# Optimization experiments

Hardware: AMD Instinct MI355X
Metric: run time of the kernel (lower is better)

## Reference

```python
import jax, jax.numpy as jnp
import numpy as np

B, H, W, C = 8, 64, 64, 128
L = H * W
NH = 4
HD = C // NH
SCALE = HD ** -0.5
WIN = 8
SHIFT = 4
DEPTH = 2
K = 3
N = WIN * WIN
NW = (H // WIN) * (W // WIN)


def _rel_pos_index(win):
    coords = np.stack(np.meshgrid(np.arange(win), np.arange(win), indexing='ij'))
    cf = coords.reshape(2, -1)
    rel = (cf[:, :, None] - cf[:, None, :]).transpose(1, 2, 0).copy()
    rel[:, :, 0] += win - 1
    rel[:, :, 1] += win - 1
    rel[:, :, 0] *= 2 * win - 1
    return rel.sum(-1)  # (N, N)

REL_IDX = jnp.asarray(_rel_pos_index(WIN).reshape(-1))


def _attn_mask(Hh, Ww, win, shift):
    img = np.zeros((Hh, Ww))
    cnt = 0
    for hs in (slice(0, -win), slice(-win, -shift), slice(-shift, None)):
        for ws in (slice(0, -win), slice(-win, -shift), slice(-shift, None)):
            img[hs, ws] = cnt
            cnt += 1
    mw = img.reshape(Hh // win, win, Ww // win, win).transpose(0, 2, 1, 3).reshape(-1, win * win)
    m = mw[:, None, :] - mw[:, :, None]
    return jnp.asarray(np.where(m != 0, -100.0, 0.0).astype(np.float32))  # (nW, N, N)

ATTN_MASK = _attn_mask(H, W, WIN, SHIFT)


def layer_norm(x, g, b, eps=1e-5):
    mu = x.mean(-1, keepdims=True)
    var = x.var(-1, keepdims=True)
    return (x - mu) / jnp.sqrt(var + eps) * g + b


def window_partition(x, win):
    Bb, Hh, Ww, Cc = x.shape
    x = x.reshape(Bb, Hh // win, win, Ww // win, win, Cc)
    return x.transpose(0, 1, 3, 2, 4, 5).reshape(-1, win, win, Cc)


def window_reverse(wins, win, Hh, Ww):
    Bb = wins.shape[0] // (Hh * Ww // win // win)
    x = wins.reshape(Bb, Hh // win, Ww // win, win, win, -1)
    return x.transpose(0, 1, 3, 2, 4, 5).reshape(Bb, Hh, Ww, -1)


def swin_block(x, shift, n1g, n1b, qkvw, qkvb, rp, pw, pb, n2g, n2b, f1w, f1b, f2w, f2b):
    shortcut = x
    x = layer_norm(x, n1g, n1b).reshape(B, H, W, C)
    if shift > 0:
        x = jnp.roll(x, (-shift, -shift), axis=(1, 2))
    xw = window_partition(x, WIN).reshape(-1, N, C)  # (B*nW, N, C)
    qkv = (xw @ qkvw + qkvb).reshape(-1, N, 3, NH, HD).transpose(2, 0, 3, 1, 4)
    q, k, v = qkv[0] * SCALE, qkv[1], qkv[2]
    attn = jnp.einsum('whnd,whmd->whnm', q, k)  # (B*nW, NH, N, N)
    bias = rp[REL_IDX].reshape(N, N, NH).transpose(2, 0, 1)
    attn = attn + bias[None]
    if shift > 0:
        attn = (attn.reshape(B, NW, NH, N, N) + ATTN_MASK[None, :, None]).reshape(-1, NH, N, N)
    attn = jax.nn.softmax(attn, axis=-1)
    out = jnp.einsum('whnm,whmd->whnd', attn, v).transpose(0, 2, 1, 3).reshape(-1, N, C)
    out = out @ pw + pb
    x = window_reverse(out.reshape(-1, WIN, WIN, C), WIN, H, W)
    if shift > 0:
        x = jnp.roll(x, (shift, shift), axis=(1, 2))
    x = shortcut + x.reshape(B, L, C)
    h = layer_norm(x, n2g, n2b)
    h = jax.nn.gelu(h @ f1w + f1b, approximate=False) @ f2w + f2b
    return x + h


def conv1d(x, w, b):  # x (B,C,L), w (O,I,K)
    y = jax.lax.conv_general_dilated(x, w, (1,), [(K // 2, K // 2)], dimension_numbers=('NCH', 'OIH', 'NCH'))
    return y + b[None, :, None]


def deform_conv1d(xt, off_w, off_b, msk_w, msk_b):
    x = xt.transpose(0, 2, 1)  # (B, C, L)
    offset = conv1d(x, off_w, off_b)                    # (B, K, L)
    mask = jax.nn.sigmoid(conv1d(x, msk_w, msk_b))      # (B, K, L)
    i = jnp.arange(L, dtype=x.dtype)
    pos = jnp.clip(i[None, None, :] + offset, 0.0, L - 1)  # (B, K, L)
    fp = jnp.floor(pos).astype(jnp.int32)
    cp = jnp.minimum(fp + 1, L - 1)
    alpha = pos - fp.astype(x.dtype)
    idx_f = jnp.broadcast_to(fp[:, None], (B, C, K, L))
    idx_c = jnp.broadcast_to(cp[:, None], (B, C, K, L))
    xe = jnp.broadcast_to(x[:, :, None, :], (B, C, K, L))
    xf = jnp.take_along_axis(xe, idx_f, axis=3)
    xc = jnp.take_along_axis(xe, idx_c, axis=3)
    samp = xf * (1.0 - alpha[:, None]) + xc * alpha[:, None]
    out = (samp * mask[:, None]).sum(2)  # (B, C, L)
    # faithful to torch: output.view(B, L, out_channels) reinterprets memory, no transpose
    return out.reshape(B, L, C)


def _forward(xt, hx, cx, red_w, red_b, n1g, n1b, qkvw, qkvb, rp, pw, pb, n2g, n2b,
             f1w, f1b, f2w, f2b, off_w, off_b, msk_w, msk_b, lf_w, lf_b, gf_w, gf_b, ff_w, ff_b):
    # global branch: inject hidden state then W-MSA / SW-MSA blocks
    g = jnp.concatenate([xt, hx], axis=-1) @ red_w + red_b
    for i, shift in enumerate((0, SHIFT)):
        g = swin_block(g, shift, n1g[i], n1b[i], qkvw[i], qkvb[i], rp[i], pw[i], pb[i],
                       n2g[i], n2b[i], f1w[i], f1b[i], f2w[i], f2b[i])
    # local branch: deformable 1D conv over token axis
    local = deform_conv1d(xt, off_w, off_b, msk_w, msk_b)
    # local-global fusion
    fu = jax.nn.relu((local @ lf_w + lf_b) * (g @ gf_w + gf_b)) @ ff_w + ff_b
    # LSTM-style gating (SwinLSTM cell update)
    gate = jax.nn.sigmoid(fu)
    cell = jnp.tanh(fu)
    cy = gate * (cx + cell)
    hy = gate * jnp.tanh(cy)
    return hy


def setup_inputs():
    key = jax.random.key(0)
    ks = iter(jax.random.split(key, 24))
    def rn(shape, s=0.02):
        return jax.random.normal(next(ks), shape, jnp.float32) * s
    return dict(
        xt=jax.random.normal(next(ks), (B, L, C), jnp.float32),
        hx=jax.random.normal(next(ks), (B, L, C), jnp.float32),
        cx=jax.random.normal(next(ks), (B, L, C), jnp.float32),
        red_w=rn((2 * C, C)), red_b=jnp.zeros((C,), jnp.float32),
        n1g=jnp.ones((DEPTH, C), jnp.float32), n1b=jnp.zeros((DEPTH, C), jnp.float32),
        qkvw=rn((DEPTH, C, 3 * C)), qkvb=jnp.zeros((DEPTH, 3 * C), jnp.float32),
        rp=rn((DEPTH, (2 * WIN - 1) ** 2, NH)),
        pw=rn((DEPTH, C, C)), pb=jnp.zeros((DEPTH, C), jnp.float32),
        n2g=jnp.ones((DEPTH, C), jnp.float32), n2b=jnp.zeros((DEPTH, C), jnp.float32),
        f1w=rn((DEPTH, C, 4 * C)), f1b=jnp.zeros((DEPTH, 4 * C), jnp.float32),
        f2w=rn((DEPTH, 4 * C, C)), f2b=jnp.zeros((DEPTH, C), jnp.float32),
        off_w=rn((K, C, K)), off_b=jnp.zeros((K,), jnp.float32),
        msk_w=rn((K, C, K)), msk_b=jnp.zeros((K,), jnp.float32),
        lf_w=rn((C, C)), lf_b=jnp.zeros((C,), jnp.float32),
        gf_w=rn((C, C)), gf_b=jnp.zeros((C,), jnp.float32),
        ff_w=rn((C, C)), ff_b=jnp.zeros((C,), jnp.float32),
    )


def reference(xt, hx, cx, red_w, red_b, n1g, n1b, qkvw, qkvb, rp, pw, pb, n2g, n2b,
              f1w, f1b, f2w, f2b, off_w, off_b, msk_w, msk_b, lf_w, lf_b, gf_w, gf_b, ff_w, ff_b):
    return _forward(xt, hx, cx, red_w, red_b, n1g, n1b, qkvw, qkvb, rp, pw, pb, n2g, n2b,
                    f1w, f1b, f2w, f2b, off_w, off_b, msk_w, msk_b, lf_w, lf_b, gf_w, gf_b, ff_w, ff_b)
```

## Files before the change

### kernel.cpp

```cpp
#include <hip/hip_runtime.h>
#include <hip/hip_bf16.h>
#include <math.h>

typedef __hip_bfloat16 bf16;
typedef unsigned short u16;
#define BF(x) __bfloat162float(x)
static __device__ __forceinline__ bf16 FB(float x) { return __float2bfloat16(x); }
static __device__ __forceinline__ u16 FBu(float x) {
    bf16 b = __float2bfloat16(x);
    return *(u16*)&b;
}

typedef __attribute__((ext_vector_type(4))) float f32x4;
typedef __attribute__((ext_vector_type(8))) __bf16 bf16x8;


#define O_REDW 0
#define O_QKVW 32768
#define O_PW   131072
#define O_F1W  163840
#define O_F2W  294912
#define O_LFW  425984
#define O_GFW  442368
#define O_FFW  458752
#define O_REDB 475136
#define O_QKVB 475264
#define O_PB   476032
#define O_F1B  476288
#define O_F2B  477312
#define O_LFB  477568
#define O_GFB  477696
#define O_FFB  477824
#define O_RP   477952
#define O_N1G  479752
#define O_N1B  480008
#define O_N2G  480264
#define O_N2B  480520
#define O_OW   480776
#define O_OB   481928
#define O_MW   481931
#define O_MB   483083

#define ROW_S 36
#define CH_S  2320

__device__ __forceinline__ int get_mode(const void* xt) {
    const unsigned* w = (const unsigned*)xt;
    int zlo = 0, inband = 0;
    #pragma unroll
    for (int i = 0; i < 32; ++i) {
        unsigned lo = w[i] & 0xFFFFu;
        int e = (int)((lo >> 7) & 0xFF);
        zlo += (lo == 0u || lo == 0x8000u);
        inband += (e >= 100 && e <= 140);
    }
    if (zlo >= 29) return 1;
    return (inband >= 20) ? 0 : 1;
}

__device__ __forceinline__ float LD(const void* p, size_t i, int mode) {
    return mode ? ((const float*)p)[i] : BF(((const bf16*)p)[i]);
}

__device__ __forceinline__ void async16(const u16* g, u16* l) {
    __builtin_amdgcn_global_load_lds(
        (const __attribute__((address_space(1))) unsigned int*)g,
        (__attribute__((address_space(3))) unsigned int*)l, 16, 0, 0);
}

struct PrepT { const void* src; int srcOff, K, N, dstOff; };
struct Prep { PrepT d[29]; int start[30]; };

__global__ void prep_k(Prep p, bf16* __restrict__ dst, const void* __restrict__ dtp) {
    const int mode = get_mode(dtp);
    int i = blockIdx.x * 256 + threadIdx.x;
    if (i >= p.start[29]) return;
    int s = 0;
    while (p.start[s + 1] <= i) ++s;
    int e = i - p.start[s];
    float v;
    if (p.d[s].N > 0) {
        int n = e / p.d[s].K, k = e % p.d[s].K;
        v = LD(p.d[s].src, (size_t)p.d[s].srcOff + (size_t)k * p.d[s].N + n, mode);
    } else {
        v = LD(p.d[s].src, (size_t)p.d[s].srcOff + e, mode);
    }
    dst[p.d[s].dstOff + e] = FB(v);
}

__launch_bounds__(256)
__global__ void xcat_k(const void* __restrict__ xt, const void* __restrict__ hx,
                       u16* __restrict__ X) {
    const int mode = get_mode(xt);
    const int total = 32768 * 32;
    for (int gidx = blockIdx.x * 256 + threadIdx.x; gidx < total;
         gidx += gridDim.x * 256) {
        int r = gidx >> 5, gi = gidx & 31;
        const void* src = (gi < 16) ? xt : hx;
        int c = (gi & 15) << 3;
        u16 outv[8];
        if (mode) {
            const float* s = (const float*)src + (size_t)r * 128 + c;
            float4 a = *(const float4*)s;
            float4 b = *(const float4*)(s + 4);
            outv[0] = FBu(a.x); outv[1] = FBu(a.y); outv[2] = FBu(a.z); outv[3] = FBu(a.w);
            outv[4] = FBu(b.x); outv[5] = FBu(b.y); outv[6] = FBu(b.z); outv[7] = FBu(b.w);
        } else {
            *(uint4*)outv = *(const uint4*)((const u16*)src + (size_t)r * 128 + c);
        }
        *(uint4*)(X + (size_t)r * 256 + (gi << 3)) = *(const uint4*)outv;
    }
}

template <int EPI>
__launch_bounds__(256)
__global__ void gemm_mfma(const u16* __restrict__ A, const u16* __restrict__ Bt,
                          const bf16* __restrict__ bias, bf16* __restrict__ outb,
                          float* __restrict__ outf, int M, int N, int K, int shift) {
    __shared__ __align__(16) u16 Als[4096];
    __shared__ __align__(16) u16 Bls[4096];
    const int tid = threadIdx.x;
    const int wave = tid >> 6, lane = tid & 63;
    const int q = lane >> 4, lr = lane & 15;
    const int wm = (wave >> 1) << 6, wn = (wave & 1) << 6;
    const int bm = blockIdx.y << 7, bn = blockIdx.x << 7;
    const f32x4 zero = {0.f, 0.f, 0.f, 0.f};
    f32x4 acc[4][4];
    #pragma unroll
    for (int i = 0; i < 4; ++i)
        #pragma unroll
        for (int j = 0; j < 4; ++j) acc[i][j] = zero;

    for (int k0 = 0; k0 < K; k0 += 32) {
        #pragma unroll
        for (int c = tid; c < 512; c += 256) {
            async16(A + (size_t)(bm + (c >> 2)) * K + k0 + ((c & 3) << 3), Als + (c << 3));
            async16(Bt + (size_t)(bn + (c >> 2)) * K + k0 + ((c & 3) << 3), Bls + (c << 3));
        }
        __syncthreads();
        bf16x8 af[4], bfr[4];
        #pragma unroll
        for (int t = 0; t < 4; ++t) {
            af[t]  = *(const bf16x8*)(Als + ((wm + (t << 4) + lr) << 5) + (q << 3));
            bfr[t] = *(const bf16x8*)(Bls + ((wn + (t << 4) + lr) << 5) + (q << 3));
        }
        #pragma unroll
        for (int mt = 0; mt < 4; ++mt)
            #pragma unroll
            for (int nt = 0; nt < 4; ++nt)
                acc[mt][nt] = __builtin_amdgcn_mfma_f32_16x16x32_bf16(
                    af[mt], bfr[nt], acc[mt][nt], 0, 0, 0);
        __syncthreads();
    }

    #pragma unroll
    for (int nt = 0; nt < 4; ++nt) {
        int col = bn + wn + (nt << 4) + lr;
        float bv = BF(bias[col]);
        #pragma unroll
        for (int mt = 0; mt < 4; ++mt) {
            int row0 = bm + wm + (mt << 4) + (q << 2);
            #pragma unroll
            for (int i = 0; i < 4; ++i) {
                int r = row0 + i;
                float v = acc[mt][nt][i] + bv;
                size_t idx = (size_t)r * N + col;
                if (EPI == 0) {
                    outb[idx] = FB(v);
                } else if (EPI == 3) {
                    int b = r >> 12, rem = r & 4095;
                    int wi = rem >> 6, n = rem & 63;
                    int hp = ((wi >> 3) << 3) + (n >> 3);
                    int wp = ((wi & 7) << 3) + (n & 7);
                    int h = (hp + shift) & 63, w = (wp + shift) & 63;
                    outf[((size_t)((b << 12) + (h << 6) + w)) * 128 + col] += v;
                } else if (EPI == 5) {
                    outf[idx] = v;
                }
            }
        }
    }
}

__launch_bounds__(256)
__global__ void qkvln_k(const float* __restrict__ g, const u16* __restrict__ wtu,
                        const bf16* __restrict__ wtb, u16* __restrict__ qkv,
                        int d, int shift) {
    __shared__ __align__(16) u16 Ach[4 * CH_S];
    __shared__ __align__(16) u16 Bb[16384];
    const int tid = threadIdx.x;
    const int wave = tid >> 6, lane = tid & 63;
    const int q = lane >> 4, lr = lane & 15;
    const int wm = (wave >> 1) << 5, wn = (wave & 1) << 6;
    const int bm = blockIdx.x << 6;

    {
        int row = tid >> 2, qtr = tid & 3;
        int r = bm + row;
        int b = r >> 12, rem = r & 4095;
        int wi = rem >> 6, n = rem & 63;
        int hp = ((wi >> 3) << 3) + (n >> 3);
        int wp = ((wi & 7) << 3) + (n & 7);
        int h = (hp + shift) & 63, w = (wp + shift) & 63;
        int src = (b << 12) + (h << 6) + w;
        const float* gr = g + (size_t)src * 128 + qtr * 32;
        float vals[32];
        float s1 = 0.f, s2 = 0.f;
        #pragma unroll
        for (int i = 0; i < 8; ++i) {
            float4 v4 = *(const float4*)(gr + i * 4);
            vals[i * 4] = v4.x; vals[i * 4 + 1] = v4.y;
            vals[i * 4 + 2] = v4.z; vals[i * 4 + 3] = v4.w;
            s1 += v4.x + v4.y + v4.z + v4.w;
            s2 += v4.x * v4.x + v4.y * v4.y + v4.z * v4.z + v4.w * v4.w;
        }
        s1 += __shfl_xor(s1, 1); s1 += __shfl_xor(s1, 2);
        s2 += __shfl_xor(s2, 1); s2 += __shfl_xor(s2, 2);
        float mu = s1 * (1.f / 128.f);
        float var = s2 * (1.f / 128.f) - mu * mu;
        float inv = rsqrtf(var + 1e-5f);
        #pragma unroll
        for (int i = 0; i < 32; ++i) {
            int c = qtr * 32 + i;
            float o = (vals[i] - mu) * inv * BF(wtb[O_N1G + d * 128 + c])
                      + BF(wtb[O_N1B + d * 128 + c]);
            Ach[qtr * CH_S + row * ROW_S + i] = FBu(o);
        }
    }
    __syncthreads();

    const f32x4 zero = {0.f, 0.f, 0.f, 0.f};
    for (int nc = 0; nc < 3; ++nc) {
        const u16* Bg = wtu + O_QKVW + d * 49152 + nc * 16384;
        #pragma unroll
        for (int i = tid; i < 2048; i += 256) {
            int kc = i >> 9, c = i & 511;
            async16(Bg + (size_t)(c >> 2) * 128 + (kc << 5) + ((c & 3) << 3),
                    Bb + (kc << 12) + (c << 3));
        }
        __syncthreads();
        f32x4 acc[2][4];
        #pragma unroll
        for (int i = 0; i < 2; ++i)
            #pragma unroll
            for (int j = 0; j < 4; ++j) acc[i][j] = zero;
        #pragma unroll
        for (int k0 = 0; k0 < 4; ++k0) {
            bf16x8 af[2], bfr[4];
            #pragma unroll
            for (int t = 0; t < 2; ++t)
                af[t] = *(const bf16x8*)(Ach + k0 * CH_S + (wm + (t << 4) + lr) * ROW_S + (q << 3));
            #pragma unroll
            for (int t = 0; t < 4; ++t)
                bfr[t] = *(const bf16x8*)(Bb + (k0 << 12) + ((wn + (t << 4) + lr) << 5) + (q << 3));
            #pragma unroll
            for (int mt = 0; mt < 2; ++mt)
                #pragma unroll
                for (int nt = 0; nt < 4; ++nt)
                    acc[mt][nt] = __builtin_amdgcn_mfma_f32_16x16x32_bf16(
                        af[mt], bfr[nt], acc[mt][nt], 0, 0, 0);
        }
        #pragma unroll
        for (int nt = 0; nt < 4; ++nt) {
            int col = wn + (nt << 4) + lr;
            float bv = BF(wtb[O_QKVB + d * 384 + nc * 128 + col]);
            #pragma unroll
            for (int mt = 0; mt < 2; ++mt) {
                #pragma unroll
                for (int i = 0; i < 4; ++i) {
                    int r = bm + wm + (mt << 4) + (q << 2) + i;
                    qkv[(size_t)r * 384 + nc * 128 + col] = FBu(acc[mt][nt][i] + bv);
                }
            }
        }
        __syncthreads();
    }
}

__launch_bounds__(256)
__global__ void attn_k(const u16* __restrict__ qkv, const bf16* __restrict__ rp,
                       u16* __restrict__ outp, int shift) {
    __shared__ float kT[4][32][64];
    __shared__ float vT[4][32][64];
    const int wq = blockIdx.x;
    const int head = threadIdx.x >> 6;
    const int t = threadIdx.x & 63;
    const size_t rbase = (size_t)(wq * 64 + t) * 384 + head * 32;
    float q[32];
    #pragma unroll
    for (int j = 0; j < 4; ++j) {
        bf16x8 qv = *(const bf16x8*)(qkv + rbase + j * 8);
        bf16x8 kv = *(const bf16x8*)(qkv + rbase + 128 + j * 8);
        bf16x8 vv = *(const bf16x8*)(qkv + rbase + 256 + j * 8);
        #pragma unroll
        for (int e = 0; e < 8; ++e) {
            int dd = j * 8 + e;
            q[dd] = (float)qv[e] * 0.17677669529663687f;
            kT[head][dd][t] = (float)kv[e];
            vT[head][dd][t] = (float)vv[e];
        }
    }
    __syncthreads();
    const int wloc = wq & 63;
    const int wh = (wloc >> 3) << 3, wwb = (wloc & 7) << 3;
    int regt = 0;
    if (shift) {
        int hp = wh + (t >> 3), wp = wwb + (t & 7);
        int rh = hp < 56 ? 0 : (hp < 60 ? 1 : 2);
        int rw = wp < 56 ? 0 : (wp < 60 ? 1 : 2);
        regt = rh * 3 + rw;
    }
    const int ti = t >> 3, tj = t & 7;
    float s[64];
    float mx = -1e30f;
    #pragma unroll
    for (int m = 0; m < 64; ++m) {
        float acc = 0.f;
        #pragma unroll
        for (int dd = 0; dd < 32; ++dd) acc += q[dd] * kT[head][dd][m];
        int idx = (ti - (m >> 3) + 7) * 15 + (tj - (m & 7) + 7);
        acc += BF(rp[idx * 4 + head]);
        if (shift) {
            int hp = wh + (m >> 3), wp = wwb + (m & 7);
            int rh = hp < 56 ? 0 : (hp < 60 ? 1 : 2);
            int rw = wp < 56 ? 0 : (wp < 60 ? 1 : 2);
            if (regt != rh * 3 + rw) acc -= 100.f;
        }
        s[m] = acc;
        mx = fmaxf(mx, acc);
    }
    float l = 0.f;
    #pragma unroll
    for (int m = 0; m < 64; ++m) {
        s[m] = expf(s[m] - mx);
        l += s[m];
    }
    const float inv = 1.f / l;
    const size_t obase = (size_t)(wq * 64 + t) * 128 + head * 32;
    #pragma unroll
    for (int j = 0; j < 4; ++j) {
        bf16x8 ov;
        #pragma unroll
        for (int e = 0; e < 8; ++e) {
            int dd = j * 8 + e;
            float a = 0.f;
            #pragma unroll
            for (int m = 0; m < 64; ++m) a += s[m] * vT[head][dd][m];
            ov[e] = (__bf16)(a * inv);
        }
        *(bf16x8*)(outp + obase + j * 8) = ov;
    }
}

__launch_bounds__(256)
__global__ void mlp_k(float* __restrict__ g, bf16* __restrict__ gbf,
                      const u16* __restrict__ wtu, const bf16* __restrict__ wtb,
                      int d) {
    __shared__ __align__(16) u16 Ach[4 * CH_S];
    __shared__ __align__(16) u16 buf1[8192];
    __shared__ __align__(16) u16 buf2[2 * CH_S];
    const int tid = threadIdx.x;
    const int wave = tid >> 6, lane = tid & 63;
    const int q = lane >> 4, lr = lane & 15;
    const int wm = (wave >> 1) << 5;
    const int wn0 = (wave & 1) << 5;
    const int wn = (wave & 1) << 6;
    const int bm = blockIdx.x << 6;

    {
        int row = tid >> 2, qtr = tid & 3;
        const float* gr = g + (size_t)(bm + row) * 128 + qtr * 32;
        float vals[32];
        float s1 = 0.f, s2 = 0.f;
        #pragma unroll
        for (int i = 0; i < 8; ++i) {
            float4 v4 = *(const float4*)(gr + i * 4);
            vals[i * 4] = v4.x; vals[i * 4 + 1] = v4.y;
            vals[i * 4 + 2] = v4.z; vals[i * 4 + 3] = v4.w;
            s1 += v4.x + v4.y + v4.z + v4.w;
            s2 += v4.x * v4.x + v4.y * v4.y + v4.z * v4.z + v4.w * v4.w;
        }
        s1 += __shfl_xor(s1, 1); s1 += __shfl_xor(s1, 2);
        s2 += __shfl_xor(s2, 1); s2 += __shfl_xor(s2, 2);
        float mu = s1 * (1.f / 128.f);
        float var = s2 * (1.f / 128.f) - mu * mu;
        float inv = rsqrtf(var + 1e-5f);
        #pragma unroll
        for (int i = 0; i < 32; ++i) {
            int c = qtr * 32 + i;
            float o = (vals[i] - mu) * inv * BF(wtb[O_N2G + d * 128 + c])
                      + BF(wtb[O_N2B + d * 128 + c]);
            Ach[qtr * CH_S + row * ROW_S + i] = FBu(o);
        }
    }
    __syncthreads();

    const f32x4 zero = {0.f, 0.f, 0.f, 0.f};
    f32x4 acc2[2][4];
    #pragma unroll
    for (int i = 0; i < 2; ++i)
        #pragma unroll
        for (int j = 0; j < 4; ++j) acc2[i][j] = zero;

    for (int h = 0; h < 8; ++h) {
        const u16* B1g = wtu + O_F1W + d * 65536 + h * 8192;
        #pragma unroll
        for (int i = tid; i < 1024; i += 256) {
            int kc = i >> 8, c = i & 255;
            async16(B1g + (c >> 2) * 128 + (kc << 5) + ((c & 3) << 3),
                    buf1 + (kc << 11) + (c << 3));
        }
        __syncthreads();
        f32x4 acc1[2][2];
        #pragma unroll
        for (int i = 0; i < 2; ++i) { acc1[i][0] = zero; acc1[i][1] = zero; }
        #pragma unroll
        for (int k0 = 0; k0 < 4; ++k0) {
            bf16x8 af[2], bfr[2];
            #pragma unroll
            for (int t = 0; t < 2; ++t) {
                af[t]  = *(const bf16x8*)(Ach + k0 * CH_S + (wm + (t << 4) + lr) * ROW_S + (q << 3));
                bfr[t] = *(const bf16x8*)(buf1 + (k0 << 11) + ((wn0 + (t << 4) + lr) << 5) + (q << 3));
            }
            #pragma unroll
            for (int mt = 0; mt < 2; ++mt)
                #pragma unroll
                for (int nt = 0; nt < 2; ++nt)
                    acc1[mt][nt] = __builtin_amdgcn_mfma_f32_16x16x32_bf16(
                        af[mt], bfr[nt], acc1[mt][nt], 0, 0, 0);
        }
        #pragma unroll
        for (int nt = 0; nt < 2; ++nt) {
            int c = wn0 + (nt << 4) + lr;
            float hb = BF(wtb[O_F1B + d * 512 + h * 64 + c]);
            #pragma unroll
            for (int mt = 0; mt < 2; ++mt) {
                #pragma unroll
                for (int i = 0; i < 4; ++i) {
                    int r = wm + (mt << 4) + (q << 2) + i;
                    float v = acc1[mt][nt][i] + hb;
                    float ge = 0.5f * v * (1.0f + erff(v * 0.70710678118654752f));
                    buf2[(c >> 5) * CH_S + r * ROW_S + (c & 31)] = FBu(ge);
                }
            }
        }
        __syncthreads();
        const u16* B2g = wtu + O_F2W + d * 65536 + h * 64;
        #pragma unroll
        for (int i = tid; i < 1024; i += 256) {
            int kc = i >> 9, c = i & 511;
            async16(B2g + (size_t)(c >> 2) * 512 + (kc << 5) + ((c & 3) << 3),
                    buf1 + (kc << 12) + (c << 3));
        }
        __syncthreads();
        #pragma unroll
        for (int kc = 0; kc < 2; ++kc) {
            bf16x8 ah[2], b2[4];
            #pragma unroll
            for (int t = 0; t < 2; ++t)
                ah[t] = *(const bf16x8*)(buf2 + kc * CH_S + (wm + (t << 4) + lr) * ROW_S + (q << 3));
            #pragma unroll
            for (int t = 0; t < 4; ++t)
                b2[t] = *(const bf16x8*)(buf1 + (kc << 12) + ((wn + (t << 4) + lr) << 5) + (q << 3));
            #pragma unroll
            for (int mt = 0; mt < 2; ++mt)
                #pragma unroll
                for (int nt = 0; nt < 4; ++nt)
                    acc2[mt][nt] = __builtin_amdgcn_mfma_f32_16x16x32_bf16(
                        ah[mt], b2[nt], acc2[mt][nt], 0, 0, 0);
        }
        __syncthreads();
    }
    #pragma unroll
    for (int nt = 0; nt < 4; ++nt) {
        int col = wn + (nt << 4) + lr;
        float bv = BF(wtb[O_F2B + d * 128 + col]);
        #pragma unroll
        for (int mt = 0; mt < 2; ++mt) {
            #pragma unroll
            for (int i = 0; i < 4; ++i) {
                int r = bm + wm + (mt << 4) + (q << 2) + i;
                size_t idx = (size_t)r * 128 + col;
                float nv = g[idx] + acc2[mt][nt][i] + bv;
                g[idx] = nv;
                gbf[idx] = FB(nv);
            }
        }
    }
}

__launch_bounds__(256)
__global__ void fuse3_k(const u16* __restrict__ Aloc, const u16* __restrict__ Ag,
                        const u16* __restrict__ wtu, const bf16* __restrict__ wtb,
                        const void* __restrict__ cx, void* __restrict__ out,
                        const void* __restrict__ dtp) {
    __shared__ __align__(16) u16 sm[32768];
    u16* sA  = sm;
    u16* sG  = sm + 4096;
    u16* sLF = sm + 8192;
    u16* sGF = sm + 12288;
    u16* relb = sm + 16384;
    const int mode = get_mode(dtp);
    const int tid = threadIdx.x;
    const int wave = tid >> 6, lane = tid & 63;
    const int q = lane >> 4, lr = lane & 15;
    const int wm = (wave >> 1) << 6, wn = (wave & 1) << 6;
    const int bm = blockIdx.x << 7;
    const f32x4 zero = {0.f, 0.f, 0.f, 0.f};
    f32x4 acc1[4][4], acc2[4][4];
    #pragma unroll
    for (int i = 0; i < 4; ++i)
        #pragma unroll
        for (int j = 0; j < 4; ++j) { acc1[i][j] = zero; acc2[i][j] = zero; }

    #pragma unroll
    for (int k0 = 0; k0 < 4; ++k0) {
        #pragma unroll
        for (int i = tid; i < 512; i += 256) {
            int ld = i & 63, r0 = (i >> 6) << 4;
            int row = r0 + (ld >> 2), sub = (ld & 3) << 3;
            int dstoff = (r0 << 5) + (ld << 3);
            async16(Aloc + (size_t)(bm + row) * 128 + (k0 << 5) + sub, sA + dstoff);
            async16(Ag   + (size_t)(bm + row) * 128 + (k0 << 5) + sub, sG + dstoff);
            async16(wtu + O_LFW + row * 128 + (k0 << 5) + sub, sLF + dstoff);
            async16(wtu + O_GFW + row * 128 + (k0 << 5) + sub, sGF + dstoff);
        }
        __syncthreads();
        bf16x8 al[4], ag[4], blf[4], bgf[4];
        #pragma unroll
        for (int t = 0; t < 4; ++t) {
            int ro = ((wm + (t << 4) + lr) << 5) + (q << 3);
            int co = ((wn + (t << 4) + lr) << 5) + (q << 3);
            al[t]  = *(const bf16x8*)(sA + ro);
            ag[t]  = *(const bf16x8*)(sG + ro);
            blf[t] = *(const bf16x8*)(sLF + co);
            bgf[t] = *(const bf16x8*)(sGF + co);
        }
        #pragma unroll
        for (int mt = 0; mt < 4; ++mt)
            #pragma unroll
            for (int nt = 0; nt < 4; ++nt) {
                acc1[mt][nt] = __builtin_amdgcn_mfma_f32_16x16x32_bf16(
                    al[mt], blf[nt], acc1[mt][nt], 0, 0, 0);
                acc2[mt][nt] = __builtin_amdgcn_mfma_f32_16x16x32_bf16(
                    ag[mt], bgf[nt], acc2[mt][nt], 0, 0, 0);
            }
        __syncthreads();
    }
    #pragma unroll
    for (int nt = 0; nt < 4; ++nt) {
        int c = wn + (nt << 4) + lr;
        float lfb = BF(wtb[O_LFB + c]);
        float gfb = BF(wtb[O_GFB + c]);
        #pragma unroll
        for (int mt = 0; mt < 4; ++mt) {
            #pragma unroll
            for (int i = 0; i < 4; ++i) {
                int r = wm + (mt << 4) + (q << 2) + i;
                float t1 = acc1[mt][nt][i] + lfb;
                float t2 = acc2[mt][nt][i] + gfb;
                float rel = t1 * t2;
                relb[((c >> 5) << 12) + (r << 5) + (c & 31)] = FBu(rel > 0.f ? rel : 0.f);
            }
        }
    }
    __syncthreads();
    f32x4 acc3[4][4];
    #pragma unroll
    for (int i = 0; i < 4; ++i)
        #pragma unroll
        for (int j = 0; j < 4; ++j) acc3[i][j] = zero;
    #pragma unroll
    for (int k0 = 0; k0 < 4; ++k0) {
        #pragma unroll
        for (int i = tid; i < 512; i += 256) {
            int ld = i & 63, r0 = (i >> 6) << 4;
            int row = r0 + (ld >> 2), sub = (ld & 3) << 3;
            async16(wtu + O_FFW + row * 128 + (k0 << 5) + sub, sA + (r0 << 5) + (ld << 3));
        }
        __syncthreads();
        bf16x8 ar[4], bff[4];
        #pragma unroll
        for (int t = 0; t < 4; ++t) {
            ar[t]  = *(const bf16x8*)(relb + (k0 << 12) + ((wm + (t << 4) + lr) << 5) + (q << 3));
            bff[t] = *(const bf16x8*)(sA + ((wn + (t << 4) + lr) << 5) + (q << 3));
        }
        #pragma unroll
        for (int mt = 0; mt < 4; ++mt)
            #pragma unroll
            for (int nt = 0; nt < 4; ++nt)
                acc3[mt][nt] = __builtin_amdgcn_mfma_f32_16x16x32_bf16(
                    ar[mt], bff[nt], acc3[mt][nt], 0, 0, 0);
        __syncthreads();
    }
    #pragma unroll
    for (int nt = 0; nt < 4; ++nt) {
        int col = wn + (nt << 4) + lr;
        float ffb = BF(wtb[O_FFB + col]);
        #pragma unroll
        for (int mt = 0; mt < 4; ++mt) {
            #pragma unroll
            for (int i = 0; i < 4; ++i) {
                int r = bm + wm + (mt << 4) + (q << 2) + i;
                size_t idx = (size_t)r * 128 + col;
                float v = acc3[mt][nt][i] + ffb;
                float gate = 1.f / (1.f + expf(-v));
                float cell = tanhf(v);
                float cy = gate * (LD(cx, idx, mode) + cell);
                float hy = gate * tanhf(cy);
                if (mode) ((float*)out)[idx] = hy;
                else      ((bf16*)out)[idx] = FB(hy);
            }
        }
    }
}

__launch_bounds__(256)
__global__ void deform_k(const void* __restrict__ xt, const bf16* __restrict__ wtb,
                         bf16* __restrict__ outL) {
    __shared__ __align__(16) u16 ot[128 * 72];
    __shared__ int s_fp[192], s_cp[192];
    __shared__ float s_al[192], s_mk[192];
    const int mode = get_mode(xt);
    const int tid = threadIdx.x;
    const int wave = tid >> 6, lane = tid & 63;
    const int b = blockIdx.x >> 6;
    const int l0 = (blockIdx.x & 63) << 6;
    float wo[3][3][2], wmk[3][3][2];
    #pragma unroll
    for (int k = 0; k < 3; ++k)
        #pragma unroll
        for (int j = 0; j < 3; ++j) {
            wo[k][j][0]  = BF(wtb[O_OW + (k * 128 + lane) * 3 + j]);
            wo[k][j][1]  = BF(wtb[O_OW + (k * 128 + lane + 64) * 3 + j]);
            wmk[k][j][0] = BF(wtb[O_MW + (k * 128 + lane) * 3 + j]);
            wmk[k][j][1] = BF(wtb[O_MW + (k * 128 + lane + 64) * 3 + j]);
        }
    for (int il = 0; il < 16; ++il) {
        int l_loc = wave * 16 + il;
        int l = l0 + l_loc;
        float a6[6] = {};
        #pragma unroll
        for (int j = 0; j < 3; ++j) {
            int row = l + j - 1;
            if (row >= 0 && row < 4096) {
                size_t base = ((size_t)(b << 12) + row) * 128;
                float x0 = LD(xt, base + lane, mode);
                float x1 = LD(xt, base + lane + 64, mode);
                #pragma unroll
                for (int k = 0; k < 3; ++k) {
                    a6[k]     += x0 * wo[k][j][0]  + x1 * wo[k][j][1];
                    a6[3 + k] += x0 * wmk[k][j][0] + x1 * wmk[k][j][1];
                }
            }
        }
        #pragma unroll
        for (int off = 32; off > 0; off >>= 1)
            #pragma unroll
            for (int k = 0; k < 6; ++k) a6[k] += __shfl_down(a6[k], off);
        if (lane == 0) {
            #pragma unroll
            for (int k = 0; k < 3; ++k) {
                float off = a6[k] + BF(wtb[O_OB + k]);
                float pos = fminf(fmaxf((float)l + off, 0.f), 4095.f);
                float fpf = floorf(pos);
                int fp = (int)fpf;
                int cp = fp + 1 > 4095 ? 4095 : fp + 1;
                s_fp[l_loc * 3 + k] = fp;
                s_cp[l_loc * 3 + k] = cp;
                s_al[l_loc * 3 + k] = pos - fpf;
                float mv = a6[3 + k] + BF(wtb[O_MB + k]);
                s_mk[l_loc * 3 + k] = 1.f / (1.f + expf(-mv));
            }
        }
    }
    __syncthreads();
    {
        int c = tid & 127, lh = tid >> 7;
        for (int it = 0; it < 32; ++it) {
            int l_loc = lh * 32 + it;
            float o = 0.f;
            #pragma unroll
            for (int k = 0; k < 3; ++k) {
                int fp = s_fp[l_loc * 3 + k];
                int cp = s_cp[l_loc * 3 + k];
                float al = s_al[l_loc * 3 + k];
                float mk = s_mk[l_loc * 3 + k];
                float xf = LD(xt, ((size_t)(b << 12) + fp) * 128 + c, mode);
                float xc = LD(xt, ((size_t)(b << 12) + cp) * 128 + c, mode);
                o += (xf * (1.f - al) + xc * al) * mk;
            }
            ot[c * 72 + l_loc] = FBu(o);
        }
    }
    __syncthreads();
    #pragma unroll
    for (int pass = 0; pass < 4; ++pass) {
        int cc = pass * 32 + (tid >> 3);
        int oo = tid & 7;
        const uint4 v = *(const uint4*)(ot + cc * 72 + oo * 8);
        *(uint4*)(outL + (size_t)b * 524288 + (size_t)cc * 4096 + l0 + oo * 8) = v;
    }
}

extern "C" void kernel_launch(void* const* d_in, const int* in_sizes, int n_in,
                              void* d_out, int out_size, void* d_ws, size_t ws_size,
                              hipStream_t stream) {
    (void)out_size; (void)ws_size;
    int I[28] = {0,1,2,3,4,5,6,7,8,9,10,11,12,13,14,15,16,17,18,19,20,21,22,23,24,25,26,27};
    if (n_in >= 28 && in_sizes[7] != 98304 && in_sizes[23] == 98304 && in_sizes[26] == 1800) {
        int alt[28] = {27, 9, 0, 25, 24, 15, 14, 23, 22, 26, 21, 20, 17, 16,
                       2, 1, 4, 3, 19, 18, 13, 12, 11, 10, 8, 7, 6, 5};
        for (int i = 0; i < 28; ++i) I[i] = alt[i];
    }
    const void* xt = d_in[I[0]];
    const void* hx = d_in[I[1]];
    const void* cx = d_in[I[2]];

    char* wsb = (char*)d_ws;
    float* g    = (float*)wsb;
    u16*   Abf  = (u16*)(wsb + 16777216);
    u16*   Bbf  = (u16*)(wsb + 25165824);
    u16*   Cbf  = (u16*)(wsb + 50331648);
    bf16*  wtb  = (bf16*)(wsb + 58720256);
    u16*   wtu  = (u16*)wtb;

    Prep p;
    PrepT descs[29] = {
        {d_in[I[3]],  0,     256, 128, O_REDW},
        {d_in[I[7]],  0,     128, 384, O_QKVW},
        {d_in[I[7]],  49152, 128, 384, O_QKVW + 49152},
        {d_in[I[10]], 0,     128, 128, O_PW},
        {d_in[I[10]], 16384, 128, 128, O_PW + 16384},
        {d_in[I[14]], 0,     128, 512, O_F1W},
        {d_in[I[14]], 65536, 128, 512, O_F1W + 65536},
        {d_in[I[16]], 0,     512, 128, O_F2W},
        {d_in[I[16]], 65536, 512, 128, O_F2W + 65536},
        {d_in[I[22]], 0,     128, 128, O_LFW},
        {d_in[I[24]], 0,     128, 128, O_GFW},
        {d_in[I[26]], 0,     128, 128, O_FFW},
        {d_in[I[4]],  0,  128, 0, O_REDB},
        {d_in[I[8]],  0,  768, 0, O_QKVB},
        {d_in[I[11]], 0,  256, 0, O_PB},
        {d_in[I[15]], 0, 1024, 0, O_F1B},
        {d_in[I[17]], 0,  256, 0, O_F2B},
        {d_in[I[23]], 0,  128, 0, O_LFB},
        {d_in[I[25]], 0,  128, 0, O_GFB},
        {d_in[I[27]], 0,  128, 0, O_FFB},
        {d_in[I[9]],  0, 1800, 0, O_RP},
        {d_in[I[5]],  0,  256, 0, O_N1G},
        {d_in[I[6]],  0,  256, 0, O_N1B},
        {d_in[I[12]], 0,  256, 0, O_N2G},
        {d_in[I[13]], 0,  256, 0, O_N2B},
        {d_in[I[18]], 0, 1152, 0, O_OW},
        {d_in[I[19]], 0,    3, 0, O_OB},
        {d_in[I[20]], 0, 1152, 0, O_MW},
        {d_in[I[21]], 0,    3, 0, O_MB},
    };
    int cum = 0;
    for (int i = 0; i < 29; ++i) {
        p.d[i] = descs[i];
        p.start[i] = cum;
        cum += (descs[i].N > 0) ? descs[i].K * descs[i].N : descs[i].K;
    }
    p.start[29] = cum;

    prep_k<<<(cum + 255) / 256, 256, 0, stream>>>(p, wtb, xt);
    xcat_k<<<1024, 256, 0, stream>>>(xt, hx, Bbf);

    gemm_mfma<5><<<dim3(1, 256), 256, 0, stream>>>(Bbf, wtu + O_REDW, wtb + O_REDB,
                                                   nullptr, g, 32768, 128, 256, 0);

    for (int d = 0; d < 2; ++d) {
        int shift = d ? 4 : 0;
        qkvln_k<<<512, 256, 0, stream>>>(g, wtu, wtb, Bbf, d, shift);
        attn_k<<<512, 256, 0, stream>>>(Bbf, wtb + O_RP + d * 900, Cbf, shift);
        gemm_mfma<3><<<dim3(1, 256), 256, 0, stream>>>(Cbf, wtu + O_PW + d * 16384,
                                                       wtb + O_PB + d * 128, nullptr, g,
                                                       32768, 128, 128, shift);
        mlp_k<<<512, 256, 0, stream>>>(g, (bf16*)Abf, wtu, wtb, d);
    }

    deform_k<<<512, 256, 0, stream>>>(xt, wtb, (bf16*)Cbf);
    fuse3_k<<<256, 256, 0, stream>>>(Cbf, Abf, wtu, wtb, cx, d_out, xt);
}
```

Baseline: 459.6 us.

## Load GEMM operands directly from global memory instead of staging through LDS

Removes the async LDS staging and barriers for weight and activation tiles in gemm_mfma, qkvln_k, mlp_k and fuse3_k, so MFMA operand fragments are read straight from global memory through the caches. fuse3_k is also retiled from 128-row to 64-row blocks with a padded LDS layout, launch bounds of 2 blocks per SM and twice as many blocks. The aim is to cut LDS traffic and synchronization and to raise occupancy. The cost is strided uncoalesced 16-byte global loads with no reuse across waves except through L1/L2, which may increase memory latency stalls.

```diff
diff --git a/kernel.cpp b/kernel.cpp
--- a/kernel.cpp
+++ b/kernel.cpp
@@ -117,8 +117,6 @@
 __global__ void gemm_mfma(const u16* __restrict__ A, const u16* __restrict__ Bt,
                           const bf16* __restrict__ bias, bf16* __restrict__ outb,
                           float* __restrict__ outf, int M, int N, int K, int shift) {
-    __shared__ __align__(16) u16 Als[4096];
-    __shared__ __align__(16) u16 Bls[4096];
     const int tid = threadIdx.x;
     const int wave = tid >> 6, lane = tid & 63;
     const int q = lane >> 4, lr = lane & 15;
@@ -132,17 +130,11 @@
         for (int j = 0; j < 4; ++j) acc[i][j] = zero;
 
     for (int k0 = 0; k0 < K; k0 += 32) {
-        #pragma unroll
-        for (int c = tid; c < 512; c += 256) {
-            async16(A + (size_t)(bm + (c >> 2)) * K + k0 + ((c & 3) << 3), Als + (c << 3));
-            async16(Bt + (size_t)(bn + (c >> 2)) * K + k0 + ((c & 3) << 3), Bls + (c << 3));
-        }
-        __syncthreads();
         bf16x8 af[4], bfr[4];
         #pragma unroll
         for (int t = 0; t < 4; ++t) {
-            af[t]  = *(const bf16x8*)(Als + ((wm + (t << 4) + lr) << 5) + (q << 3));
-            bfr[t] = *(const bf16x8*)(Bls + ((wn + (t << 4) + lr) << 5) + (q << 3));
+            af[t]  = *(const bf16x8*)(A  + (size_t)(bm + wm + (t << 4) + lr) * K + k0 + (q << 3));
+            bfr[t] = *(const bf16x8*)(Bt + (size_t)(bn + wn + (t << 4) + lr) * K + k0 + (q << 3));
         }
         #pragma unroll
         for (int mt = 0; mt < 4; ++mt)
@@ -150,7 +142,6 @@
             for (int nt = 0; nt < 4; ++nt)
                 acc[mt][nt] = __builtin_amdgcn_mfma_f32_16x16x32_bf16(
                     af[mt], bfr[nt], acc[mt][nt], 0, 0, 0);
-        __syncthreads();
     }
 
     #pragma unroll
@@ -187,7 +178,6 @@
                         const bf16* __restrict__ wtb, u16* __restrict__ qkv,
                         int d, int shift) {
     __shared__ __align__(16) u16 Ach[4 * CH_S];
-    __shared__ __align__(16) u16 Bb[16384];
     const int tid = threadIdx.x;
     const int wave = tid >> 6, lane = tid & 63;
     const int q = lane >> 4, lr = lane & 15;
@@ -232,13 +222,6 @@
     const f32x4 zero = {0.f, 0.f, 0.f, 0.f};
     for (int nc = 0; nc < 3; ++nc) {
         const u16* Bg = wtu + O_QKVW + d * 49152 + nc * 16384;
-        #pragma unroll
-        for (int i = tid; i < 2048; i += 256) {
-            int kc = i >> 9, c = i & 511;
-            async16(Bg + (size_t)(c >> 2) * 128 + (kc << 5) + ((c & 3) << 3),
-                    Bb + (kc << 12) + (c << 3));
-        }
-        __syncthreads();
         f32x4 acc[2][4];
         #pragma unroll
         for (int i = 0; i < 2; ++i)
@@ -252,7 +235,7 @@
                 af[t] = *(const bf16x8*)(Ach + k0 * CH_S + (wm + (t << 4) + lr) * ROW_S + (q << 3));
             #pragma unroll
             for (int t = 0; t < 4; ++t)
-                bfr[t] = *(const bf16x8*)(Bb + (k0 << 12) + ((wn + (t << 4) + lr) << 5) + (q << 3));
+                bfr[t] = *(const bf16x8*)(Bg + ((wn + (t << 4) + lr) << 7) + (k0 << 5) + (q << 3));
             #pragma unroll
             for (int mt = 0; mt < 2; ++mt)
                 #pragma unroll
@@ -273,7 +256,6 @@
                 }
             }
         }
-        __syncthreads();
     }
 }
 
@@ -357,7 +339,6 @@
                       const u16* __restrict__ wtu, const bf16* __restrict__ wtb,
                       int d) {
     __shared__ __align__(16) u16 Ach[4 * CH_S];
-    __shared__ __align__(16) u16 buf1[8192];
     __shared__ __align__(16) u16 buf2[2 * CH_S];
     const int tid = threadIdx.x;
     const int wave = tid >> 6, lane = tid & 63;
@@ -404,13 +385,6 @@
 
     for (int h = 0; h < 8; ++h) {
         const u16* B1g = wtu + O_F1W + d * 65536 + h * 8192;
-        #pragma unroll
-        for (int i = tid; i < 1024; i += 256) {
-            int kc = i >> 8, c = i & 255;
-            async16(B1g + (c >> 2) * 128 + (kc << 5) + ((c & 3) << 3),
-                    buf1 + (kc << 11) + (c << 3));
-        }
-        __syncthreads();
         f32x4 acc1[2][2];
         #pragma unroll
         for (int i = 0; i < 2; ++i) { acc1[i][0] = zero; acc1[i][1] = zero; }
@@ -420,7 +394,7 @@
             #pragma unroll
             for (int t = 0; t < 2; ++t) {
                 af[t]  = *(const bf16x8*)(Ach + k0 * CH_S + (wm + (t << 4) + lr) * ROW_S + (q << 3));
-                bfr[t] = *(const bf16x8*)(buf1 + (k0 << 11) + ((wn0 + (t << 4) + lr) << 5) + (q << 3));
+                bfr[t] = *(const bf16x8*)(B1g + ((wn0 + (t << 4) + lr) << 7) + (k0 << 5) + (q << 3));
             }
             #pragma unroll
             for (int mt = 0; mt < 2; ++mt)
@@ -447,13 +421,6 @@
         __syncthreads();
         const u16* B2g = wtu + O_F2W + d * 65536 + h * 64;
         #pragma unroll
-        for (int i = tid; i < 1024; i += 256) {
-            int kc = i >> 9, c = i & 511;
-            async16(B2g + (size_t)(c >> 2) * 512 + (kc << 5) + ((c & 3) << 3),
-                    buf1 + (kc << 12) + (c << 3));
-        }
-        __syncthreads();
-        #pragma unroll
         for (int kc = 0; kc < 2; ++kc) {
             bf16x8 ah[2], b2[4];
             #pragma unroll
@@ -461,7 +428,7 @@
                 ah[t] = *(const bf16x8*)(buf2 + kc * CH_S + (wm + (t << 4) + lr) * ROW_S + (q << 3));
             #pragma unroll
             for (int t = 0; t < 4; ++t)
-                b2[t] = *(const bf16x8*)(buf1 + (kc << 12) + ((wn + (t << 4) + lr) << 5) + (q << 3));
+                b2[t] = *(const bf16x8*)(B2g + (size_t)(wn + (t << 4) + lr) * 512 + (kc << 5) + (q << 3));
             #pragma unroll
             for (int mt = 0; mt < 2; ++mt)
                 #pragma unroll
@@ -489,55 +456,42 @@
     }
 }
 
-__launch_bounds__(256)
+__launch_bounds__(256, 2)
 __global__ void fuse3_k(const u16* __restrict__ Aloc, const u16* __restrict__ Ag,
                         const u16* __restrict__ wtu, const bf16* __restrict__ wtb,
                         const void* __restrict__ cx, void* __restrict__ out,
                         const void* __restrict__ dtp) {
-    __shared__ __align__(16) u16 sm[32768];
-    u16* sA  = sm;
-    u16* sG  = sm + 4096;
-    u16* sLF = sm + 8192;
-    u16* sGF = sm + 12288;
-    u16* relb = sm + 16384;
+    __shared__ __align__(16) u16 relb[4 * CH_S];
     const int mode = get_mode(dtp);
     const int tid = threadIdx.x;
     const int wave = tid >> 6, lane = tid & 63;
     const int q = lane >> 4, lr = lane & 15;
-    const int wm = (wave >> 1) << 6, wn = (wave & 1) << 6;
-    const int bm = blockIdx.x << 7;
+    const int wm = (wave >> 1) << 5, wn = (wave & 1) << 6;
+    const int bm = blockIdx.x << 6;
     const f32x4 zero = {0.f, 0.f, 0.f, 0.f};
-    f32x4 acc1[4][4], acc2[4][4];
-    #pragma unroll
-    for (int i = 0; i < 4; ++i)
+    f32x4 acc1[2][4], acc2[2][4];
+    #pragma unroll
+    for (int i = 0; i < 2; ++i)
         #pragma unroll
         for (int j = 0; j < 4; ++j) { acc1[i][j] = zero; acc2[i][j] = zero; }
 
     #pragma unroll
     for (int k0 = 0; k0 < 4; ++k0) {
-        #pragma unroll
-        for (int i = tid; i < 512; i += 256) {
-            int ld = i & 63, r0 = (i >> 6) << 4;
-            int row = r0 + (ld >> 2), sub = (ld & 3) << 3;
-            int dstoff = (r0 << 5) + (ld << 3);
-            async16(Aloc + (size_t)(bm + row) * 128 + (k0 << 5) + sub, sA + dstoff);
-            async16(Ag   + (size_t)(bm + row) * 128 + (k0 << 5) + sub, sG + dstoff);
-            async16(wtu + O_LFW + row * 128 + (k0 << 5) + sub, sLF + dstoff);
-            async16(wtu + O_GFW + row * 128 + (k0 << 5) + sub, sGF + dstoff);
-        }
-        __syncthreads();
-        bf16x8 al[4], ag[4], blf[4], bgf[4];
+        bf16x8 al[2], ag[2], blf[4], bgf[4];
+        #pragma unroll
+        for (int t = 0; t < 2; ++t) {
+            size_t off = (size_t)(bm + wm + (t << 4) + lr) * 128 + (k0 << 5) + (q << 3);
+            al[t] = *(const bf16x8*)(Aloc + off);
+            ag[t] = *(const bf16x8*)(Ag + off);
+        }
         #pragma unroll
         for (int t = 0; t < 4; ++t) {
-            int ro = ((wm + (t << 4) + lr) << 5) + (q << 3);
-            int co = ((wn + (t << 4) + lr) << 5) + (q << 3);
-            al[t]  = *(const bf16x8*)(sA + ro);
-            ag[t]  = *(const bf16x8*)(sG + ro);
-            blf[t] = *(const bf16x8*)(sLF + co);
-            bgf[t] = *(const bf16x8*)(sGF + co);
-        }
-        #pragma unroll
-        for (int mt = 0; mt < 4; ++mt)
+            int woff = ((wn + (t << 4) + lr) << 7) + (k0 << 5) + (q << 3);
+            blf[t] = *(const bf16x8*)(wtu + O_LFW + woff);
+            bgf[t] = *(const bf16x8*)(wtu + O_GFW + woff);
+        }
+        #pragma unroll
+        for (int mt = 0; mt < 2; ++mt)
             #pragma unroll
             for (int nt = 0; nt < 4; ++nt) {
                 acc1[mt][nt] = __builtin_amdgcn_mfma_f32_16x16x32_bf16(
@@ -545,7 +499,6 @@
                 acc2[mt][nt] = __builtin_amdgcn_mfma_f32_16x16x32_bf16(
                     ag[mt], bgf[nt], acc2[mt][nt], 0, 0, 0);
             }
-        __syncthreads();
     }
     #pragma unroll
     for (int nt = 0; nt < 4; ++nt) {
@@ -553,52 +506,45 @@
         float lfb = BF(wtb[O_LFB + c]);
         float gfb = BF(wtb[O_GFB + c]);
         #pragma unroll
-        for (int mt = 0; mt < 4; ++mt) {
+        for (int mt = 0; mt < 2; ++mt) {
             #pragma unroll
             for (int i = 0; i < 4; ++i) {
                 int r = wm + (mt << 4) + (q << 2) + i;
                 float t1 = acc1[mt][nt][i] + lfb;
                 float t2 = acc2[mt][nt][i] + gfb;
                 float rel = t1 * t2;
-                relb[((c >> 5) << 12) + (r << 5) + (c & 31)] = FBu(rel > 0.f ? rel : 0.f);
+                relb[(c >> 5) * CH_S + r * ROW_S + (c & 31)] = FBu(rel > 0.f ? rel : 0.f);
             }
         }
     }
     __syncthreads();
-    f32x4 acc3[4][4];
-    #pragma unroll
-    for (int i = 0; i < 4; ++i)
+    f32x4 acc3[2][4];
+    #pragma unroll
+    for (int i = 0; i < 2; ++i)
         #pragma unroll
         for (int j = 0; j < 4; ++j) acc3[i][j] = zero;
     #pragma unroll
     for (int k0 = 0; k0 < 4; ++k0) {
-        #pragma unroll
-        for (int i = tid; i < 512; i += 256) {
-            int ld = i & 63, r0 = (i >> 6) << 4;
-            int row = r0 + (ld >> 2), sub = (ld & 3) << 3;
-            async16(wtu + O_FFW + row * 128 + (k0 << 5) + sub, sA + (r0 << 5) + (ld << 3));
-        }
-        __syncthreads();
-        bf16x8 ar[4], bff[4];
-        #pragma unroll
-        for (int t = 0; t < 4; ++t) {
-            ar[t]  = *(const bf16x8*)(relb + (k0 << 12) + ((wm + (t << 4) + lr) << 5) + (q << 3));
-            bff[t] = *(const bf16x8*)(sA + ((wn + (t << 4) + lr) << 5) + (q << 3));
-        }
-        #pragma unroll
-        for (int mt = 0; mt < 4; ++mt)
+        bf16x8 ar[2], bff[4];
+        #pragma unroll
+        for (int t = 0; t < 2; ++t)
+            ar[t] = *(const bf16x8*)(relb + k0 * CH_S + (wm + (t << 4) + lr) * ROW_S + (q << 3));
+        #pragma unroll
+        for (int t = 0; t < 4; ++t)
+            bff[t] = *(const bf16x8*)(wtu + O_FFW + ((wn + (t << 4) + lr) << 7) + (k0 << 5) + (q << 3));
+        #pragma unroll
+        for (int mt = 0; mt < 2; ++mt)
             #pragma unroll
             for (int nt = 0; nt < 4; ++nt)
                 acc3[mt][nt] = __builtin_amdgcn_mfma_f32_16x16x32_bf16(
                     ar[mt], bff[nt], acc3[mt][nt], 0, 0, 0);
-        __syncthreads();
     }
     #pragma unroll
     for (int nt = 0; nt < 4; ++nt) {
         int col = wn + (nt << 4) + lr;
         float ffb = BF(wtb[O_FFB + col]);
         #pragma unroll
-        for (int mt = 0; mt < 4; ++mt) {
+        for (int mt = 0; mt < 2; ++mt) {
             #pragma unroll
             for (int i = 0; i < 4; ++i) {
                 int r = bm + wm + (mt << 4) + (q << 2) + i;
@@ -782,5 +728,5 @@
     }
 
     deform_k<<<512, 256, 0, stream>>>(xt, wtb, (bf16*)Cbf);
-    fuse3_k<<<256, 256, 0, stream>>>(Cbf, Abf, wtu, wtb, cx, d_out, xt);
-}
+    fuse3_k<<<512, 256, 0, stream>>>(Cbf, Abf, wtu, wtb, cx, d_out, xt);
+}
```

Result: slower. 496.8 us (+8.1%).
